# Kernel optimization log

Hardware: AMD Instinct MI355X
Metric: run time of the kernel (lower is better)

The kernel has to match this reference:

```python
import jax, jax.numpy as jnp
import numpy as np

B, T = 256, 256
D_TEXT, D_AUDIO, D_VISION = 300, 74, 35
D = D_TEXT + D_AUDIO + D_VISION  # 409
H = 1024
CELL = 512
OUT = 1


def setup_inputs() -> dict:
    key = jax.random.key(0)
    ks = jax.random.split(key, 8)
    s_ih = 1.0 / np.sqrt(H)
    return {
        "x_text": jax.random.normal(ks[0], (B, T, D_TEXT), jnp.float32),
        "x_audio": jax.random.normal(ks[1], (B, T, D_AUDIO), jnp.float32),
        "x_vision": jax.random.normal(ks[2], (B, T, D_VISION), jnp.float32),
        "W_ih": jax.random.normal(ks[3], (4 * H, D), jnp.float32) * s_ih,
        "W_hh": jax.random.normal(ks[4], (4 * H, H), jnp.float32) * s_ih,
        "b_ih": jnp.zeros((4 * H,), jnp.float32),
        "b_hh": jnp.zeros((4 * H,), jnp.float32),
        "W1": jax.random.normal(ks[5], (CELL, H), jnp.float32) / np.sqrt(H),
        "b1": jnp.zeros((CELL,), jnp.float32),
        "W2": jax.random.normal(ks[6], (OUT, CELL), jnp.float32) / np.sqrt(CELL),
        "b2": jnp.zeros((OUT,), jnp.float32),
    }


def _lstm_mlp(x_text, x_audio, x_vision, W_ih, W_hh, b_ih, b_hh, W1, b1, W2, b2):
    # concat modalities along feature dim: [B, T, D]
    x = jnp.concatenate([x_text, x_audio, x_vision], axis=2)
    b = x.shape[0]
    h0 = jnp.zeros((b, H), x.dtype)
    c0 = jnp.zeros((b, H), x.dtype)
    # precompute input-to-gate projection for all timesteps: [T, B, 4H]
    xg = jnp.einsum('btd,gd->tbg', x, W_ih) + (b_ih + b_hh)

    def step(carry, xg_t):
        h, c = carry
        gates = xg_t + h @ W_hh.T  # [B, 4H]
        i, f, g, o = jnp.split(gates, 4, axis=-1)  # PyTorch LSTMCell gate order
        i = jax.nn.sigmoid(i)
        f = jax.nn.sigmoid(f)
        g = jnp.tanh(g)
        o = jax.nn.sigmoid(o)
        c = f * c + i * g
        h = o * jnp.tanh(c)
        return (h, c), None

    (h_last, _), _ = jax.lax.scan(step, (h0, c0), xg)
    # SimpleNet: Linear -> ReLU -> Dropout(eval: identity) -> Linear
    hidden = jax.nn.relu(h_last @ W1.T + b1)
    return hidden @ W2.T + b2  # [B, OUT]


def reference(x_text, x_audio, x_vision, W_ih, W_hh, b_ih, b_hh, W1, b1, W2, b2):
    return _lstm_mlp(x_text, x_audio, x_vision, W_ih, W_hh, b_ih, b_hh, W1, b1, W2, b2)
```

## Files before the change

kernel.cpp:

```cpp
#include <hip/hip_runtime.h>
#include <cstdint>
#include <cstddef>


typedef __attribute__((ext_vector_type(8))) short short8;
typedef __attribute__((ext_vector_type(4))) float f32x4;

#define MFMA_BF16(A,B,C) __builtin_amdgcn_mfma_f32_16x16x32_bf16((A),(B),(C),0,0,0)

#define OFF_FLAGS 0u
#define OFF_HBUF0 4096u
#define OFF_CBUF  528384u
#define ZERO_SPAN 1576960u
#define OFF_HBUF1 1576960u
#define OFF_HFIN  2101248u
#define OFF_HID   3149824u
#define OFF_BIAS  3674112u
#define OFF_WHH   3690496u
#define OFF_WIH   12079104u
#define OFF_XB    15486976u
#define OFF_XG    70012928u
#define WS_NEED   137121792ull

static __device__ __forceinline__ uint16_t f2bf(float f) {
  uint32_t u = __builtin_bit_cast(uint32_t, f);
  uint32_t r = u + 0x7FFFu + ((u >> 16) & 1u);
  return (uint16_t)(r >> 16);
}
static __device__ __forceinline__ float bf2f_lo(uint32_t u) {
  return __builtin_bit_cast(float, u << 16);
}
static __device__ __forceinline__ float bf2f_hi(uint32_t u) {
  return __builtin_bit_cast(float, u & 0xFFFF0000u);
}
static __device__ __forceinline__ float sigm(float x) {
  return 1.0f / (1.0f + __expf(-x));
}
static __device__ __forceinline__ float tanh_f(float x) {
  float e = __expf(2.0f * x);
  return 1.0f - 2.0f / (e + 1.0f);
}
static __device__ __forceinline__ void gld_lds16_coh(const void* gsrc, void* ldst) {
  __builtin_amdgcn_global_load_lds(
      (const __attribute__((address_space(1))) uint32_t*)gsrc,
      (__attribute__((address_space(3))) uint32_t*)ldst, 16, 0, 0x11);
}

__global__ __launch_bounds__(256) void pack_xb_kernel(
    const float* __restrict__ xt, const float* __restrict__ xa,
    const float* __restrict__ xv, uint16_t* __restrict__ xb)
{
  int id = blockIdx.x * 256 + threadIdx.x;
  int lane = id & 63;
  int rem  = id >> 6;
  int ks = rem % 13;
  int mt = rem / 13;
  int m = mt * 16 + (lane & 15);
  int t = m >> 8;
  int b = m & 255;
  int k0 = ks * 32 + (lane >> 4) * 8;
  size_t base = (size_t)b * 256 + t;
  uint16_t vals[8];
#pragma unroll
  for (int e = 0; e < 8; ++e) {
    int k = k0 + e;
    float v;
    if (k < 300)      v = xt[base * 300 + k];
    else if (k < 374) v = xa[base * 74  + (k - 300)];
    else if (k < 409) v = xv[base * 35  + (k - 374)];
    else              v = 0.0f;
    vals[e] = f2bf(v);
  }
  uint32_t* d32 = (uint32_t*)(xb + (size_t)id * 8);
#pragma unroll
  for (int i = 0; i < 4; ++i)
    d32[i] = (uint32_t)vals[2*i] | ((uint32_t)vals[2*i+1] << 16);
}

__global__ __launch_bounds__(256) void pack_whh_kernel(
    const float* __restrict__ whh, uint16_t* __restrict__ wp)
{
  int id = blockIdx.x * 256 + threadIdx.x;
  int lane = id & 63;
  int ks = (id >> 6) & 31;
  int q  = (id >> 11) & 3;
  int s  = id >> 13;
  int row = q * 1024 + s * 16 + (lane & 15);
  int k0 = ks * 32 + (lane >> 4) * 8;
  const float* src = whh + (size_t)row * 1024 + k0;
  uint16_t vals[8];
#pragma unroll
  for (int e = 0; e < 8; ++e) vals[e] = f2bf(src[e]);
  uint32_t* d32 = (uint32_t*)(wp + (size_t)id * 8);
#pragma unroll
  for (int i = 0; i < 4; ++i)
    d32[i] = (uint32_t)vals[2*i] | ((uint32_t)vals[2*i+1] << 16);
}

__global__ __launch_bounds__(256) void pack_wih_kernel(
    const float* __restrict__ wih, uint16_t* __restrict__ wp)
{
  int id = blockIdx.x * 256 + threadIdx.x;
  int lane = id & 63;
  int rem = id >> 6;
  int ks = rem % 13;
  int nt = rem / 13;
  int n = nt * 16 + (lane & 15);
  int k0 = ks * 32 + (lane >> 4) * 8;
  uint16_t vals[8];
#pragma unroll
  for (int e = 0; e < 8; ++e) {
    int k = k0 + e;
    vals[e] = (k < 409) ? f2bf(wih[(size_t)n * 409 + k]) : (uint16_t)0;
  }
  uint32_t* d32 = (uint32_t*)(wp + (size_t)id * 8);
#pragma unroll
  for (int i = 0; i < 4; ++i)
    d32[i] = (uint32_t)vals[2*i] | ((uint32_t)vals[2*i+1] << 16);
}

__global__ __launch_bounds__(256) void pack_bias_kernel(
    const float* __restrict__ b_ih, const float* __restrict__ b_hh,
    float* __restrict__ bias)
{
  int id = blockIdx.x * 256 + threadIdx.x;
  bias[id] = b_ih[id] + b_hh[id];
}

__global__ __launch_bounds__(256) void xg_gemm_kernel(
    const short8* __restrict__ xb, const short8* __restrict__ wih,
    const float* __restrict__ bias, uint2* __restrict__ xg, int chunk)
{
  int tid = threadIdx.x;
  int lane = tid & 63;
  int w = tid >> 6;
  int wm = w & 1, wn = w >> 1;
  int bm = blockIdx.x, bn = blockIdx.y;
  int mtb = bm * 8 + wm * 4;
  int ntb = bn * 8 + wn * 4;
  int col = lane & 15;

  f32x4 acc[4][4];
#pragma unroll
  for (int b = 0; b < 4; ++b) {
    float bv = bias[(ntb + b) * 16 + col];
    f32x4 v = {bv, bv, bv, bv};
#pragma unroll
    for (int a = 0; a < 4; ++a) acc[a][b] = v;
  }
  size_t mt_glob = (size_t)chunk * 512 + mtb;
  for (int ks = 0; ks < 13; ++ks) {
    short8 Af[4], Bf[4];
#pragma unroll
    for (int a = 0; a < 4; ++a)
      Af[a] = xb[((mt_glob + a) * 13 + ks) * 64 + lane];
#pragma unroll
    for (int b = 0; b < 4; ++b)
      Bf[b] = wih[(((size_t)(ntb + b)) * 13 + ks) * 64 + lane];
#pragma unroll
    for (int a = 0; a < 4; ++a)
#pragma unroll
      for (int b = 0; b < 4; ++b)
        acc[a][b] = MFMA_BF16(Af[a], Bf[b], acc[a][b]);
  }
#pragma unroll
  for (int a = 0; a < 4; ++a) {
    int mt = mtb + a;
    int t_loc = mt >> 4;
    int bt = mt & 15;
#pragma unroll
    for (int b = 0; b < 4; ++b) {
      size_t idx = (((size_t)t_loc * 256 + (ntb + b)) * 16 + bt) * 64 + lane;
      f32x4 v = acc[a][b];
      uint2 o;
      o.x = (uint32_t)f2bf(v[0]) | ((uint32_t)f2bf(v[1]) << 16);
      o.y = (uint32_t)f2bf(v[2]) | ((uint32_t)f2bf(v[3]) << 16);
      xg[idx] = o;
    }
  }
}

__global__ __launch_bounds__(256, 1) void scan_kernel(
    const uint16_t* __restrict__ whh_p, const uint2* __restrict__ xg,
    uint16_t* __restrict__ hbuf0, uint16_t* __restrict__ hbuf1,
    float* __restrict__ c_buf, float* __restrict__ h_final,
    uint32_t* flags, int chunk)
{
  extern __shared__ char smem[];
  float* gl = (float*)(smem + 131072);

  const int tid = threadIdx.x;
  const int bid = blockIdx.x;
  const int g = bid >> 6, s = bid & 63;
  const int lane = tid & 63, w = tid >> 6;
  const int mw = w & 1, nw = w >> 1;

  const short8* wsrc = (const short8*)whh_p + (size_t)s * 4 * 32 * 64;
  const short8* w0p = wsrc + ((size_t)(nw * 2 + 0) * 32) * 64 + lane;
  const short8* w1p = wsrc + ((size_t)(nw * 2 + 1) * 32) * 64 + lane;

  const int row_e = tid >> 2;
  const int j_e = (tid & 3) * 4;
  const int R_e = g * 64 + row_e;
  const int col_e = s * 16 + j_e;
  f32x4 c4 = *(const f32x4*)(c_buf + (size_t)R_e * 1024 + col_e);

  size_t hstore_base;
  {
    int cg0 = col_e;
    int ksh = cg0 >> 5, quad = (cg0 >> 3) & 3, e0 = cg0 & 7;
    int mth = row_e >> 4;
    int laneh = quad * 16 + (row_e & 15);
    hstore_base = (((size_t)(g * 4 + mth) * 32 + ksh) * 64 + laneh) * 8 + e0;
  }

  const short8* Afrag = (const short8*)smem;
  const int myflag = g * 64 + (tid & 63);

  uint2 xp[2][2];
#pragma unroll
  for (int a = 0; a < 2; ++a)
#pragma unroll
    for (int b = 0; b < 2; ++b) {
      int q = nw * 2 + b;
      size_t idx = (((size_t)0 * 256 + (q * 64 + s)) * 16 + (g * 4 + mw * 2 + a)) * 64 + lane;
      xp[a][b] = xg[idx];
    }

  for (int l = 0; l < 32; ++l) {
    const int ts = chunk * 32 + l;
    const uint16_t* hin = (ts & 1) ? hbuf1 : hbuf0;
    uint16_t* hout = (ts & 1) ? hbuf0 : hbuf1;

    {
      const uint16_t* gbase = hin + (size_t)g * 65536
                              + (size_t)(w * 32) * 512 + (size_t)lane * 8;
      char* lbase = smem + (size_t)(w * 32) * 1024;
#pragma unroll
      for (int p = 0; p < 32; ++p)
        gld_lds16_coh(gbase + (size_t)p * 512, lbase + p * 1024);
    }

    f32x4 acc[2][2];
#pragma unroll
    for (int a = 0; a < 2; ++a)
#pragma unroll
      for (int b = 0; b < 2; ++b) {
        uint2 p = xp[a][b];
        f32x4 v = {bf2f_lo(p.x), bf2f_hi(p.x), bf2f_lo(p.y), bf2f_hi(p.y)};
        acc[a][b] = v;
      }

    __syncthreads();

#pragma unroll
    for (int ks = 0; ks < 32; ++ks) {
      short8 B0 = w0p[ks * 64];
      short8 B1 = w1p[ks * 64];
      short8 A0 = Afrag[((mw * 2 + 0) * 32 + ks) * 64 + lane];
      short8 A1 = Afrag[((mw * 2 + 1) * 32 + ks) * 64 + lane];
      acc[0][0] = MFMA_BF16(A0, B0, acc[0][0]);
      acc[0][1] = MFMA_BF16(A0, B1, acc[0][1]);
      acc[1][0] = MFMA_BF16(A1, B0, acc[1][0]);
      acc[1][1] = MFMA_BF16(A1, B1, acc[1][1]);
    }

    {
      int r0 = (lane >> 4) * 4;
      int cc = lane & 15;
#pragma unroll
      for (int a = 0; a < 2; ++a)
#pragma unroll
        for (int b = 0; b < 2; ++b) {
          int row = (mw * 2 + a) * 16 + r0;
          int colc = (nw * 2 + b) * 16 + cc;
#pragma unroll
          for (int r = 0; r < 4; ++r)
            gl[(row + r) * 68 + colc] = acc[a][b][r];
        }
    }
    __syncthreads();
    float hv[4];
#pragma unroll
    for (int u = 0; u < 4; ++u) {
      int cj = j_e + u;
      float xi = gl[row_e * 68 + cj];
      float xf = gl[row_e * 68 + 16 + cj];
      float xg_ = gl[row_e * 68 + 32 + cj];
      float xo = gl[row_e * 68 + 48 + cj];
      float cn = sigm(xf) * c4[u] + sigm(xi) * tanh_f(xg_);
      c4[u] = cn;
      hv[u] = sigm(xo) * tanh_f(cn);
    }
    {
      uint32_t w0 = (uint32_t)f2bf(hv[0]) | ((uint32_t)f2bf(hv[1]) << 16);
      uint32_t w1 = (uint32_t)f2bf(hv[2]) | ((uint32_t)f2bf(hv[3]) << 16);
      unsigned long long v = ((unsigned long long)w1 << 32) | w0;
      __hip_atomic_store((unsigned long long*)(hout + hstore_base), v,
                         __ATOMIC_RELAXED, __HIP_MEMORY_SCOPE_AGENT);
    }
    if (chunk == 7 && l == 31) {
      f32x4 hh = {hv[0], hv[1], hv[2], hv[3]};
      *(f32x4*)(h_final + (size_t)R_e * 1024 + col_e) = hh;
    }
    if (l != 31) {
      __syncthreads();
      if (tid == 0) {
        __hip_atomic_store(&flags[bid], (uint32_t)(ts + 1),
                           __ATOMIC_RELAXED, __HIP_MEMORY_SCOPE_AGENT);
      }
      {
        int ln = l + 1;
#pragma unroll
        for (int a = 0; a < 2; ++a)
#pragma unroll
          for (int b = 0; b < 2; ++b) {
            int q = nw * 2 + b;
            size_t idx = (((size_t)ln * 256 + (q * 64 + s)) * 16 + (g * 4 + mw * 2 + a)) * 64 + lane;
            xp[a][b] = xg[idx];
          }
      }
      while (__hip_atomic_load(&flags[myflag], __ATOMIC_RELAXED,
                               __HIP_MEMORY_SCOPE_AGENT) < (uint32_t)(ts + 1)) {
        __builtin_amdgcn_s_sleep(1);
      }
      __syncthreads();
    }
  }
  *(f32x4*)(c_buf + (size_t)R_e * 1024 + col_e) = c4;
}

__global__ __launch_bounds__(256) void mlp1_kernel(
    const float* __restrict__ h_final, const float* __restrict__ W1,
    const float* __restrict__ b1, float* __restrict__ hidden)
{
  __shared__ float hl[8 * 1024];
  __shared__ float part[4 * 64 * 8];
  int tid = threadIdx.x;
  int rb = blockIdx.x;
  int cb = blockIdx.y;
  const f32x4* hsrc = (const f32x4*)(h_final + (size_t)rb * 8 * 1024);
  for (int i = tid; i < 2048; i += 256) ((f32x4*)hl)[i] = hsrc[i];
  __syncthreads();
  int cell_l = tid & 63;
  int kq = tid >> 6;
  int cell = cb * 64 + cell_l;
  float accv[8] = {0,0,0,0,0,0,0,0};
  const f32x4* wrow = (const f32x4*)(W1 + (size_t)cell * 1024) + kq * 64;
  const f32x4* hl4 = (const f32x4*)hl;
  for (int k4 = 0; k4 < 64; ++k4) {
    f32x4 wv = wrow[k4];
    int kidx = kq * 64 + k4;
#pragma unroll
    for (int r = 0; r < 8; ++r) {
      f32x4 hv = hl4[r * 256 + kidx];
      accv[r] += wv[0] * hv[0] + wv[1] * hv[1] + wv[2] * hv[2] + wv[3] * hv[3];
    }
  }
#pragma unroll
  for (int r = 0; r < 8; ++r) part[(kq * 64 + cell_l) * 8 + r] = accv[r];
  __syncthreads();
#pragma unroll
  for (int rr = 0; rr < 2; ++rr) {
    int r = kq * 2 + rr;
    float sum = b1[cell];
    for (int q = 0; q < 4; ++q) sum += part[(q * 64 + cell_l) * 8 + r];
    hidden[(size_t)(rb * 8 + r) * 512 + cell] = fmaxf(sum, 0.0f);
  }
}

__global__ __launch_bounds__(256) void mlp2_kernel(
    const float* __restrict__ hidden, const float* __restrict__ W2,
    const float* __restrict__ b2, float* __restrict__ out)
{
  __shared__ float w2l[512];
  int tid = threadIdx.x;
  for (int i = tid; i < 512; i += 256) w2l[i] = W2[i];
  __syncthreads();
  const f32x4* hrow = (const f32x4*)(hidden + (size_t)tid * 512);
  const f32x4* w4 = (const f32x4*)w2l;
  float acc = b2[0];
  for (int k = 0; k < 128; ++k) {
    f32x4 a = hrow[k], b = w4[k];
    acc += a[0] * b[0] + a[1] * b[1] + a[2] * b[2] + a[3] * b[3];
  }
  out[tid] = acc;
}

extern "C" void kernel_launch(void* const* d_in, const int* in_sizes, int n_in,
                              void* d_out, int out_size, void* d_ws, size_t ws_size,
                              hipStream_t stream)
{
  (void)in_sizes; (void)n_in; (void)out_size;
  if (ws_size < WS_NEED) return;

  const float* xt   = (const float*)d_in[0];
  const float* xa   = (const float*)d_in[1];
  const float* xv   = (const float*)d_in[2];
  const float* W_ih = (const float*)d_in[3];
  const float* W_hh = (const float*)d_in[4];
  const float* b_ih = (const float*)d_in[5];
  const float* b_hh = (const float*)d_in[6];
  const float* W1   = (const float*)d_in[7];
  const float* b1   = (const float*)d_in[8];
  const float* W2   = (const float*)d_in[9];
  const float* b2   = (const float*)d_in[10];
  float* out = (float*)d_out;
  char* ws = (char*)d_ws;

  uint32_t* flags   = (uint32_t*)(ws + OFF_FLAGS);
  uint16_t* hb0     = (uint16_t*)(ws + OFF_HBUF0);
  uint16_t* hb1     = (uint16_t*)(ws + OFF_HBUF1);
  float*    c_buf   = (float*)(ws + OFF_CBUF);
  float*    h_final = (float*)(ws + OFF_HFIN);
  float*    hidden  = (float*)(ws + OFF_HID);
  float*    bias    = (float*)(ws + OFF_BIAS);
  uint16_t* whh_p   = (uint16_t*)(ws + OFF_WHH);
  uint16_t* wih_p   = (uint16_t*)(ws + OFF_WIH);
  uint16_t* xb      = (uint16_t*)(ws + OFF_XB);
  uint2*    xg      = (uint2*)(ws + OFF_XG);

  hipFuncSetAttribute((const void*)scan_kernel,
                      hipFuncAttributeMaxDynamicSharedMemorySize, 148480);

  hipMemsetAsync(ws, 0, ZERO_SPAN, stream);

  pack_xb_kernel  <<<13312, 256, 0, stream>>>(xt, xa, xv, xb);
  pack_whh_kernel <<<2048,  256, 0, stream>>>(W_hh, whh_p);
  pack_wih_kernel <<<832,   256, 0, stream>>>(W_ih, wih_p);
  pack_bias_kernel<<<16,    256, 0, stream>>>(b_ih, b_hh, bias);

  for (int c = 0; c < 8; ++c) {
    xg_gemm_kernel<<<dim3(64, 32), 256, 0, stream>>>(
        (const short8*)xb, (const short8*)wih_p, bias, xg, c);
    scan_kernel<<<256, 256, 148480, stream>>>(
        whh_p, xg, hb0, hb1, c_buf, h_final, flags, c);
  }
  mlp1_kernel<<<dim3(32, 8), 256, 0, stream>>>(h_final, W1, b1, hidden);
  mlp2_kernel<<<1, 256, 0, stream>>>(hidden, W2, b2, out);
}
```

Before: 2.223 ms.

## Give each wave all four gates for its rows, dropping the LDS gate exchange

```diff
diff --git a/kernel.cpp b/kernel.cpp
--- a/kernel.cpp
+++ b/kernel.cpp
@@ -187,45 +187,33 @@
     uint32_t* flags, int chunk)
 {
   extern __shared__ char smem[];
-  float* gl = (float*)(smem + 131072);
 
   const int tid = threadIdx.x;
   const int bid = blockIdx.x;
   const int g = bid >> 6, s = bid & 63;
   const int lane = tid & 63, w = tid >> 6;
-  const int mw = w & 1, nw = w >> 1;
-
-  const short8* wsrc = (const short8*)whh_p + (size_t)s * 4 * 32 * 64;
-  const short8* w0p = wsrc + ((size_t)(nw * 2 + 0) * 32) * 64 + lane;
-  const short8* w1p = wsrc + ((size_t)(nw * 2 + 1) * 32) * 64 + lane;
-
-  const int row_e = tid >> 2;
-  const int j_e = (tid & 3) * 4;
-  const int R_e = g * 64 + row_e;
-  const int col_e = s * 16 + j_e;
-  f32x4 c4 = *(const f32x4*)(c_buf + (size_t)R_e * 1024 + col_e);
-
-  size_t hstore_base;
-  {
-    int cg0 = col_e;
-    int ksh = cg0 >> 5, quad = (cg0 >> 3) & 3, e0 = cg0 & 7;
-    int mth = row_e >> 4;
-    int laneh = quad * 16 + (row_e & 15);
-    hstore_base = (((size_t)(g * 4 + mth) * 32 + ksh) * 64 + laneh) * 8 + e0;
-  }
-
-  const short8* Afrag = (const short8*)smem;
-  const int myflag = g * 64 + (tid & 63);
-
-  uint2 xp[2][2];
-#pragma unroll
-  for (int a = 0; a < 2; ++a)
-#pragma unroll
-    for (int b = 0; b < 2; ++b) {
-      int q = nw * 2 + b;
-      size_t idx = (((size_t)0 * 256 + (q * 64 + s)) * 16 + (g * 4 + mw * 2 + a)) * 64 + lane;
-      xp[a][b] = xg[idx];
-    }
+
+  const short8* wsrc = (const short8*)(whh_p + (size_t)s * 65536);
+
+  f32x4* cslot = (f32x4*)c_buf + ((size_t)bid * 4 + w) * 64 + lane;
+  f32x4 c4 = *cslot;
+
+  const int r0 = (lane >> 4) * 4;
+  const int cc = lane & 15;
+
+  const int kk = 16 * s + cc;
+  const int ksh = kk >> 5;
+  const int quad = (kk >> 3) & 3;
+  const int ee = kk & 7;
+  const size_t hslab = ((size_t)(g * 4 + w) * 32 + ksh) * 64;
+
+  const short8* Afrag = (const short8*)(smem + w * 32768);
+  const int myflag = g * 64 + lane;
+
+  uint2 xp[4];
+#pragma unroll
+  for (int q = 0; q < 4; ++q)
+    xp[q] = xg[(((size_t)0 * 256 + (q * 64 + s)) * 16 + (g * 4 + w)) * 64 + lane];
 
   for (int l = 0; l < 32; ++l) {
     const int ts = chunk * 32 + l;
@@ -233,75 +221,57 @@
     uint16_t* hout = (ts & 1) ? hbuf0 : hbuf1;
 
     {
-      const uint16_t* gbase = hin + (size_t)g * 65536
-                              + (size_t)(w * 32) * 512 + (size_t)lane * 8;
-      char* lbase = smem + (size_t)(w * 32) * 1024;
+      const uint16_t* gbase = hin + ((size_t)(g * 4 + w) * 32 * 64 + lane) * 8;
+      char* lbase = smem + w * 32768;
 #pragma unroll
       for (int p = 0; p < 32; ++p)
         gld_lds16_coh(gbase + (size_t)p * 512, lbase + p * 1024);
     }
 
-    f32x4 acc[2][2];
-#pragma unroll
-    for (int a = 0; a < 2; ++a)
-#pragma unroll
-      for (int b = 0; b < 2; ++b) {
-        uint2 p = xp[a][b];
-        f32x4 v = {bf2f_lo(p.x), bf2f_hi(p.x), bf2f_lo(p.y), bf2f_hi(p.y)};
-        acc[a][b] = v;
+    f32x4 acc[4];
+#pragma unroll
+    for (int q = 0; q < 4; ++q) {
+      uint2 p = xp[q];
+      f32x4 v = {bf2f_lo(p.x), bf2f_hi(p.x), bf2f_lo(p.y), bf2f_hi(p.y)};
+      acc[q] = v;
+    }
+
+    __syncthreads();
+
+#pragma unroll
+    for (int ks = 0; ks < 32; ++ks) {
+      short8 A = Afrag[ks * 64 + lane];
+      acc[0] = MFMA_BF16(A, wsrc[(ks) * 64 + lane], acc[0]);
+      acc[1] = MFMA_BF16(A, wsrc[(32 + ks) * 64 + lane], acc[1]);
+      acc[2] = MFMA_BF16(A, wsrc[(64 + ks) * 64 + lane], acc[2]);
+      acc[3] = MFMA_BF16(A, wsrc[(96 + ks) * 64 + lane], acc[3]);
+    }
+
+    float hv[4];
+#pragma unroll
+    for (int rg = 0; rg < 4; ++rg) {
+      float cn = sigm(acc[1][rg]) * c4[rg] + sigm(acc[0][rg]) * tanh_f(acc[2][rg]);
+      c4[rg] = cn;
+      hv[rg] = sigm(acc[3][rg]) * tanh_f(cn);
+    }
+
+#pragma unroll
+    for (int rg = 0; rg < 4; ++rg) {
+      uint32_t v = (uint32_t)f2bf(hv[rg]);
+      uint32_t w0 = v | ((uint32_t)__shfl_xor((int)v, 1, 64) << 16);
+      uint32_t w1 = (uint32_t)__shfl_xor((int)w0, 2, 64);
+      if ((lane & 3) == 0) {
+        unsigned long long v64 =
+            (unsigned long long)w0 | ((unsigned long long)w1 << 32);
+        size_t slot = (hslab + (size_t)(quad * 16 + r0 + rg)) * 8 + ee;
+        __hip_atomic_store((unsigned long long*)(hout + slot), v64,
+                           __ATOMIC_RELAXED, __HIP_MEMORY_SCOPE_AGENT);
       }
-
-    __syncthreads();
-
-#pragma unroll
-    for (int ks = 0; ks < 32; ++ks) {
-      short8 B0 = w0p[ks * 64];
-      short8 B1 = w1p[ks * 64];
-      short8 A0 = Afrag[((mw * 2 + 0) * 32 + ks) * 64 + lane];
-      short8 A1 = Afrag[((mw * 2 + 1) * 32 + ks) * 64 + lane];
-      acc[0][0] = MFMA_BF16(A0, B0, acc[0][0]);
-      acc[0][1] = MFMA_BF16(A0, B1, acc[0][1]);
-      acc[1][0] = MFMA_BF16(A1, B0, acc[1][0]);
-      acc[1][1] = MFMA_BF16(A1, B1, acc[1][1]);
-    }
-
-    {
-      int r0 = (lane >> 4) * 4;
-      int cc = lane & 15;
-#pragma unroll
-      for (int a = 0; a < 2; ++a)
-#pragma unroll
-        for (int b = 0; b < 2; ++b) {
-          int row = (mw * 2 + a) * 16 + r0;
-          int colc = (nw * 2 + b) * 16 + cc;
-#pragma unroll
-          for (int r = 0; r < 4; ++r)
-            gl[(row + r) * 68 + colc] = acc[a][b][r];
-        }
-    }
-    __syncthreads();
-    float hv[4];
-#pragma unroll
-    for (int u = 0; u < 4; ++u) {
-      int cj = j_e + u;
-      float xi = gl[row_e * 68 + cj];
-      float xf = gl[row_e * 68 + 16 + cj];
-      float xg_ = gl[row_e * 68 + 32 + cj];
-      float xo = gl[row_e * 68 + 48 + cj];
-      float cn = sigm(xf) * c4[u] + sigm(xi) * tanh_f(xg_);
-      c4[u] = cn;
-      hv[u] = sigm(xo) * tanh_f(cn);
-    }
-    {
-      uint32_t w0 = (uint32_t)f2bf(hv[0]) | ((uint32_t)f2bf(hv[1]) << 16);
-      uint32_t w1 = (uint32_t)f2bf(hv[2]) | ((uint32_t)f2bf(hv[3]) << 16);
-      unsigned long long v = ((unsigned long long)w1 << 32) | w0;
-      __hip_atomic_store((unsigned long long*)(hout + hstore_base), v,
-                         __ATOMIC_RELAXED, __HIP_MEMORY_SCOPE_AGENT);
     }
     if (chunk == 7 && l == 31) {
-      f32x4 hh = {hv[0], hv[1], hv[2], hv[3]};
-      *(f32x4*)(h_final + (size_t)R_e * 1024 + col_e) = hh;
+#pragma unroll
+      for (int rg = 0; rg < 4; ++rg)
+        h_final[(size_t)(g * 64 + w * 16 + r0 + rg) * 1024 + 16 * s + cc] = hv[rg];
     }
     if (l != 31) {
       __syncthreads();
@@ -312,22 +282,16 @@
       {
         int ln = l + 1;
 #pragma unroll
-        for (int a = 0; a < 2; ++a)
-#pragma unroll
-          for (int b = 0; b < 2; ++b) {
-            int q = nw * 2 + b;
-            size_t idx = (((size_t)ln * 256 + (q * 64 + s)) * 16 + (g * 4 + mw * 2 + a)) * 64 + lane;
-            xp[a][b] = xg[idx];
-          }
+        for (int q = 0; q < 4; ++q)
+          xp[q] = xg[(((size_t)ln * 256 + (q * 64 + s)) * 16 + (g * 4 + w)) * 64 + lane];
       }
       while (__hip_atomic_load(&flags[myflag], __ATOMIC_RELAXED,
                                __HIP_MEMORY_SCOPE_AGENT) < (uint32_t)(ts + 1)) {
         __builtin_amdgcn_s_sleep(1);
       }
-      __syncthreads();
-    }
-  }
-  *(f32x4*)(c_buf + (size_t)R_e * 1024 + col_e) = c4;
+    }
+  }
+  *cslot = c4;
 }
 
 __global__ __launch_bounds__(256) void mlp1_kernel(
@@ -421,7 +385,7 @@
   uint2*    xg      = (uint2*)(ws + OFF_XG);
 
   hipFuncSetAttribute((const void*)scan_kernel,
-                      hipFuncAttributeMaxDynamicSharedMemorySize, 148480);
+                      hipFuncAttributeMaxDynamicSharedMemorySize, 131072);
 
   hipMemsetAsync(ws, 0, ZERO_SPAN, stream);
 
@@ -433,7 +397,7 @@
   for (int c = 0; c < 8; ++c) {
     xg_gemm_kernel<<<dim3(64, 32), 256, 0, stream>>>(
         (const short8*)xb, (const short8*)wih_p, bias, xg, c);
-    scan_kernel<<<256, 256, 148480, stream>>>(
+    scan_kernel<<<256, 256, 131072, stream>>>(
         whh_p, xg, hb0, hb1, c_buf, h_final, flags, c);
   }
   mlp1_kernel<<<dim3(32, 8), 256, 0, stream>>>(h_final, W1, b1, hidden);
```

Result: slower. 3.386 ms (+52.3%).
